# Optimization experiments

Measured on AMD Instinct MI355X. Metric: run time of the kernel, lower is better.

The kernel has to match this reference:

```python
import jax, jax.numpy as jnp
import numpy as np

N, HID, K = 256, 64, 2
B, T_ENC, T_DEC = 64, 12, 12
IN_DIM, OUT_DIM = 2, 1
NUM_SUPPORTS = 2
M = NUM_SUPPORTS * K + 1  # identity + K hops per support


def setup_inputs() -> dict:
    key = jax.random.key(0)
    ks = jax.random.split(key, 16)

    def w(k, shape, scale=0.05):
        return jax.random.normal(k, shape, dtype=jnp.float32) * scale

    def support(k):
        S = jax.random.uniform(k, (N, N), dtype=jnp.float32)
        return S / jnp.sum(S, axis=1, keepdims=True)  # random-walk normalized

    F0e = IN_DIM + HID   # encoder layer-0 concat(input, hidden) feature dim
    F1 = HID + HID       # layer-1 feature dim
    F0d = OUT_DIM + HID  # decoder layer-0 feature dim
    return {
        "encoder_inputs": jax.random.normal(ks[0], (B, T_ENC, N, IN_DIM), dtype=jnp.float32),
        "decoder_inputs": jax.random.normal(ks[1], (B, T_DEC, N, OUT_DIM), dtype=jnp.float32),
        "support0": support(ks[2]),
        "support1": support(ks[3]),
        "enc0_Wg": w(ks[4], (F0e, M, 2 * HID)), "enc0_bg": jnp.ones((2 * HID,), jnp.float32),
        "enc0_Wc": w(ks[5], (F0e, M, HID)),     "enc0_bc": jnp.zeros((HID,), jnp.float32),
        "enc1_Wg": w(ks[6], (F1, M, 2 * HID)),  "enc1_bg": jnp.ones((2 * HID,), jnp.float32),
        "enc1_Wc": w(ks[7], (F1, M, HID)),      "enc1_bc": jnp.zeros((HID,), jnp.float32),
        "dec0_Wg": w(ks[8], (F0d, M, 2 * HID)), "dec0_bg": jnp.ones((2 * HID,), jnp.float32),
        "dec0_Wc": w(ks[9], (F0d, M, HID)),     "dec0_bc": jnp.zeros((HID,), jnp.float32),
        "dec1_Wg": w(ks[10], (F1, M, 2 * HID)), "dec1_bg": jnp.ones((2 * HID,), jnp.float32),
        "dec1_Wc": w(ks[11], (F1, M, HID)),     "dec1_bc": jnp.zeros((HID,), jnp.float32),
        "proj_W": w(ks[12], (HID, OUT_DIM), 0.1),
        "proj_b": jnp.zeros((OUT_DIM,), jnp.float32),
    }


def _diff_conv(supports, x, h, W, b, in_dim):
    # x: (B, N*in_dim), h: (B, N*HID), W: (F, M, O) matching torch flatten order (f*M+m)
    Bsz = x.shape[0]
    xs = jnp.concatenate([x.reshape(Bsz, N, in_dim), h.reshape(Bsz, N, HID)], axis=-1)
    mats = [xs]
    for S in supports:
        x0 = xs
        x1 = jnp.einsum('mn,bnf->bmf', S, xs)
        mats.append(x1)
        for _ in range(2, K + 1):
            x2 = 2.0 * jnp.einsum('mn,bnf->bmf', S, x1) - x0  # Chebyshev recurrence
            mats.append(x2)
            x1, x0 = x2, x1
    X = jnp.stack(mats, axis=2)  # (B, N, M, F)
    out = jnp.einsum('bnmf,fmo->bno', X, W) + b
    return out.reshape(Bsz, -1)


def _cell(supports, x, h, Wg, bg, Wc, bc, in_dim):
    # DCGRUCell: sigmoid gates from diffusion conv, tanh candidate, GRU update
    Bsz = x.shape[0]
    ru = jax.nn.sigmoid(_diff_conv(supports, x, h, Wg, bg, in_dim)).reshape(Bsz, N, 2 * HID)
    r = ru[..., :HID].reshape(Bsz, N * HID)
    u = ru[..., HID:].reshape(Bsz, N * HID)
    c = jnp.tanh(_diff_conv(supports, x, r * h, Wc, bc, in_dim))
    return u * h + (1.0 - u) * c


def _forward(encoder_inputs, decoder_inputs, support0, support1,
             enc0_Wg, enc0_bg, enc0_Wc, enc0_bc, enc1_Wg, enc1_bg, enc1_Wc, enc1_bc,
             dec0_Wg, dec0_bg, dec0_Wc, dec0_bc, dec1_Wg, dec1_bg, dec1_Wc, dec1_bc,
             proj_W, proj_b):
    sup = (support0, support1)
    Bsz = encoder_inputs.shape[0]
    # encoder: (B,T,N,D) -> (T,B,N*D); zero initial hidden
    cur = jnp.transpose(encoder_inputs, (1, 0, 2, 3)).reshape(T_ENC, Bsz, N * IN_DIM)
    enc_params = [(enc0_Wg, enc0_bg, enc0_Wc, enc0_bc, IN_DIM),
                  (enc1_Wg, enc1_bg, enc1_Wc, enc1_bc, HID)]
    h_enc = []
    for (Wg, bg, Wc, bc, ind) in enc_params:
        h0 = jnp.zeros((Bsz, N * HID), cur.dtype)
        def estep(h, x, Wg=Wg, bg=bg, Wc=Wc, bc=bc, ind=ind):
            hn = _cell(sup, x, h, Wg, bg, Wc, bc, ind)
            return hn, hn
        hT, cur = jax.lax.scan(estep, h0, cur)
        h_enc.append(hT)
    # decoder (eval mode: no teacher forcing, dropout off); go symbol = zeros
    dec_params = [(dec0_Wg, dec0_bg, dec0_Wc, dec0_bc, OUT_DIM),
                  (dec1_Wg, dec1_bg, dec1_Wc, dec1_bc, HID)]
    go = jnp.zeros((Bsz, N * OUT_DIM), cur.dtype)

    def dstep(carry, _):
        hs, cur_in = carry
        out = cur_in
        new_hs = []
        for i, (Wg, bg, Wc, bc, ind) in enumerate(dec_params):
            hn = _cell(sup, out, hs[i], Wg, bg, Wc, bc, ind)
            out = hn
            new_hs.append(hn)
        proj = (jnp.einsum('bnh,ho->bno', out.reshape(Bsz, N, HID), proj_W) + proj_b)
        proj = proj.reshape(Bsz, N * OUT_DIM)
        return ((new_hs[0], new_hs[1]), proj), proj

    _, outs = jax.lax.scan(dstep, ((h_enc[0], h_enc[1]), go), None, length=T_DEC)
    outs = outs.reshape(T_DEC, Bsz, N, OUT_DIM)
    return jnp.transpose(outs, (1, 0, 2, 3))  # (B, T_DEC, N, OUT_DIM)


def reference(encoder_inputs, decoder_inputs, support0, support1,
              enc0_Wg, enc0_bg, enc0_Wc, enc0_bc, enc1_Wg, enc1_bg, enc1_Wc, enc1_bc,
              dec0_Wg, dec0_bg, dec0_Wc, dec0_bc, dec1_Wg, dec1_bg, dec1_Wc, dec1_bc,
              proj_W, proj_b):
    return _forward(encoder_inputs, decoder_inputs, support0, support1,
                    enc0_Wg, enc0_bg, enc0_Wc, enc0_bc, enc1_Wg, enc1_bg, enc1_Wc, enc1_bc,
                    dec0_Wg, dec0_bg, dec0_Wc, dec0_bc, dec1_Wg, dec1_bg, dec1_Wc, dec1_bc,
                    proj_W, proj_b)
```

## Files before the change

### kernel.cpp

```cpp
#include <hip/hip_runtime.h>
#include <stdint.h>


typedef short short8 __attribute__((ext_vector_type(8)));
typedef float f32x4 __attribute__((ext_vector_type(4)));
typedef unsigned short ushort4v __attribute__((ext_vector_type(4)));
typedef unsigned long long u64;
typedef u64 u64x2 __attribute__((ext_vector_type(2)));

#define DEVI __device__ __forceinline__

DEVI unsigned short f2bf(float x) {
  unsigned int u = __builtin_bit_cast(unsigned int, x);
  u += 0x7FFFu + ((u >> 16) & 1u);
  return (unsigned short)(u >> 16);
}
DEVI u64 ald(const u64* p) { return __hip_atomic_load(p, __ATOMIC_RELAXED, __HIP_MEMORY_SCOPE_AGENT); }
DEVI void ast(u64* p, u64 v) { __hip_atomic_store(p, v, __ATOMIC_RELAXED, __HIP_MEMORY_SCOPE_AGENT); }
DEVI float aldf(const float* p) { return __hip_atomic_load(p, __ATOMIC_RELAXED, __HIP_MEMORY_SCOPE_AGENT); }
DEVI void astf(float* p, float v) { __hip_atomic_store(p, v, __ATOMIC_RELAXED, __HIP_MEMORY_SCOPE_AGENT); }

struct KP {
  const float* enc_in;
  const float* sup0; const float* sup1;
  const float* Wsrc[8];
  const float* bias[8];
  const float* prW; const float* prB;
  float* out;
  unsigned short* A;
  unsigned short* Wp[8];
  unsigned short* H0[2];
  unsigned short* H1[2];
  unsigned short* RH0;
  unsigned short* RH1;
  float* XD;
  unsigned* ctr;
};

__global__ void prep(KP p) {
  const int i = blockIdx.x, tid = threadIdx.x;
  {
    const int s = i & 1, r = i >> 1;
    const float* S = s ? p.sup1 : p.sup0;
    float acc = 0.f;
    for (int k = 0; k < 256; ++k) acc = fmaf(S[r * 256 + k], S[k * 256 + tid], acc);
    p.A[(2 * s + 0) * 65536 + r * 256 + tid] = f2bf(S[r * 256 + tid]);
    p.A[(2 * s + 1) * 65536 + r * 256 + tid] = f2bf(2.f * acc - (r == tid ? 1.f : 0.f));
  }
  {
    const int gtid = i * 256 + tid;
    const int Fs[8]  = {66, 66, 128, 128, 65, 65, 128, 128};
    const int Os[8]  = {128, 64, 128, 64, 128, 64, 128, 64};
    const int FPs[8] = {96, 96, 128, 128, 96, 96, 128, 128};
    for (int w = 0; w < 8; ++w) {
      const int FPw = FPs[w], KPw = 5 * FPw, tot = Os[w] * KPw;
      for (int e = gtid; e < tot; e += 512 * 256) {
        const int o = e / KPw, k2 = e - o * KPw, m = k2 / FPw, f = k2 - m * FPw;
        p.Wp[w][e] = f2bf((f < Fs[w]) ? p.Wsrc[w][(f * 5 + m) * Os[w] + o] : 0.f);
      }
    }
  }
  {
    const int gtid = i * 256 + tid;
    u64* z0 = (u64*)p.H0[0];
    u64* z1 = (u64*)p.H1[0];
    ast(z0 + 2 * gtid, 0); ast(z0 + 2 * gtid + 1, 0);
    ast(z1 + 2 * gtid, 0); ast(z1 + 2 * gtid + 1, 0);
  }
  if (i == 0 && tid < 64)
    __hip_atomic_store(p.ctr + tid * 64, 0u, __ATOMIC_RELAXED, __HIP_MEMORY_SCOPE_AGENT);
}

template<int IND, int FP, int MODE, bool XSTAGE>
DEVI void dc_stage(int b, int n0, int tid,
                   const float* xf32,
                   const unsigned short* xbf,
                   const unsigned short* hrows,
                   const unsigned short* Amats,
                   const unsigned short* Wp, const float* bias,
                   f32x4 (&hreg)[2], f32x4 (&ureg)[2],
                   unsigned short* grows,
                   const float* projW, const float* projB,
                   float* outp, float* xdout,
                   unsigned short* xsT, unsigned short* Hbuf)
{
  constexpr int O = (MODE == 0) ? 128 : 64;
  constexpr int KPW = 5 * FP;
  constexpr int XS = 264;
  constexpr int HS = 136;
  constexpr int NFT = FP / 16;
  constexpr int NOT_ = O / 16;
  constexpr int FT_W = (NFT + 3) / 4;
  constexpr int OT_W = (NOT_ + 3) / 4;

  const int wv8 = tid >> 6, ln = tid & 63;
  const int l15 = ln & 15, l4 = ln >> 4;
  const int wr = wv8 & 1, wc = wv8 >> 1;
  const int r0 = wr * 32;

  {
    u64 la[4], lb[4];
    const u64* src = (const u64*)hrows;
#pragma unroll
    for (int it = 0; it < 4; ++it) {
      const int g = tid + it * 512;
      la[it] = ald(src + 2 * g); lb[it] = ald(src + 2 * g + 1);
    }
#pragma unroll
    for (int it = 0; it < 4; ++it) {
      const int g = tid + it * 512, row = g >> 5, c = g & 31;
      u64x2 v; v[0] = la[it]; v[1] = lb[it];
      *reinterpret_cast<u64x2*>(&xsT[(IND + row) * XS + c * 8]) = v;
    }
  }
  if (XSTAGE) {
    if (IND == 64) {
      u64 la[4], lb[4];
      const u64* src = (const u64*)xbf;
#pragma unroll
      for (int it = 0; it < 4; ++it) {
        const int g = tid + it * 512;
        la[it] = ald(src + 2 * g); lb[it] = ald(src + 2 * g + 1);
      }
#pragma unroll
      for (int it = 0; it < 4; ++it) {
        const int g = tid + it * 512, row = g >> 5, c = g & 31;
        u64x2 v; v[0] = la[it]; v[1] = lb[it];
        *reinterpret_cast<u64x2*>(&xsT[row * XS + c * 8]) = v;
      }
    } else if (IND == 2) {
      const float v = xf32[tid];
      xsT[(tid & 1) * XS + (tid >> 1)] = f2bf(v);
    } else {
      if (tid < 256) xsT[tid] = xf32 ? f2bf(aldf(xf32 + tid)) : (unsigned short)0;
    }
  }
  __syncthreads();
#pragma unroll
  for (int it = 0; it < FP / 8; ++it) {
    const int e = tid + it * 512, f = e >> 6, nl = e & 63;
    Hbuf[nl * HS + f] = xsT[f * XS + n0 + nl];
  }
  __syncthreads();

  f32x4 pacc[2][OT_W];
#pragma unroll
  for (int rt = 0; rt < 2; ++rt)
#pragma unroll
    for (int oi = 0; oi < OT_W; ++oi) pacc[rt][oi] = 0.f;

  auto proj_step = [&](int m) {
#pragma unroll
    for (int k0 = 0; k0 < FP; k0 += 32) {
      short8 af[2];
#pragma unroll
      for (int rt = 0; rt < 2; ++rt)
        af[rt] = *reinterpret_cast<const short8*>(&Hbuf[(r0 + rt * 16 + l15) * HS + k0 + l4 * 8]);
#pragma unroll
      for (int oi = 0; oi < OT_W; ++oi) {
        const int ot = wc + 4 * oi;
        if (ot < NOT_) {
          short8 bf = *reinterpret_cast<const short8*>(&Wp[(ot * 16 + l15) * KPW + m * FP + k0 + l4 * 8]);
#pragma unroll
          for (int rt = 0; rt < 2; ++rt)
            pacc[rt][oi] = __builtin_amdgcn_mfma_f32_16x16x32_bf16(af[rt], bf, pacc[rt][oi], 0, 0, 0);
        }
      }
    }
  };

  proj_step(0);

  for (int mi = 0; mi < 4; ++mi) {
    const unsigned short* Am = Amats + mi * 65536;
    f32x4 hacc[2][FT_W];
#pragma unroll
    for (int rt = 0; rt < 2; ++rt)
#pragma unroll
      for (int fi = 0; fi < FT_W; ++fi) hacc[rt][fi] = 0.f;

#pragma unroll
    for (int k0 = 0; k0 < 256; k0 += 32) {
      short8 af[2];
#pragma unroll
      for (int rt = 0; rt < 2; ++rt)
        af[rt] = *reinterpret_cast<const short8*>(&Am[(n0 + r0 + rt * 16 + l15) * 256 + k0 + l4 * 8]);
#pragma unroll
      for (int fi = 0; fi < FT_W; ++fi) {
        const int ft = wc + 4 * fi;
        if (ft < NFT) {
          short8 bf = *reinterpret_cast<const short8*>(&xsT[(ft * 16 + l15) * XS + k0 + l4 * 8]);
#pragma unroll
          for (int rt = 0; rt < 2; ++rt)
            hacc[rt][fi] = __builtin_amdgcn_mfma_f32_16x16x32_bf16(af[rt], bf, hacc[rt][fi], 0, 0, 0);
        }
      }
    }
    __syncthreads();
#pragma unroll
    for (int fi = 0; fi < FT_W; ++fi) {
      const int ft = wc + 4 * fi;
      if (ft < NFT) {
#pragma unroll
        for (int rt = 0; rt < 2; ++rt)
#pragma unroll
          for (int j = 0; j < 4; ++j)
            Hbuf[(r0 + rt * 16 + l4 * 4 + j) * HS + ft * 16 + l15] = f2bf(hacc[rt][fi][j]);
      }
    }
    __syncthreads();
    proj_step(mi + 1);
  }

  if (MODE == 0) {
    const float br = bias[wc * 16 + l15];
    const float bu = bias[64 + wc * 16 + l15];
#pragma unroll
    for (int rt = 0; rt < 2; ++rt) {
      f32x4 uu;
      ushort4v pk;
#pragma unroll
      for (int jj = 0; jj < 4; ++jj) {
        const float r = 1.f / (1.f + __expf(-(pacc[rt][0][jj] + br)));
        uu[jj] = 1.f / (1.f + __expf(-(pacc[rt][1][jj] + bu)));
        pk[jj] = f2bf(r * hreg[rt][jj]);
      }
      ureg[rt] = uu;
      ast((u64*)(grows + (wc * 16 + l15) * 256 + n0 + r0 + rt * 16 + l4 * 4),
          __builtin_bit_cast(u64, pk));
    }
  } else {
    float* hrow = reinterpret_cast<float*>(Hbuf);
    if (MODE == 2) __syncthreads();
    const float bc = bias[wc * 16 + l15];
#pragma unroll
    for (int rt = 0; rt < 2; ++rt) {
      f32x4 hn;
      ushort4v pk;
#pragma unroll
      for (int jj = 0; jj < 4; ++jj) {
        const float ex = __expf(2.f * (pacc[rt][0][jj] + bc));
        const float c = 1.f - 2.f / (ex + 1.f);
        hn[jj] = ureg[rt][jj] * hreg[rt][jj] + (1.f - ureg[rt][jj]) * c;
        pk[jj] = f2bf(hn[jj]);
      }
      hreg[rt] = hn;
      ast((u64*)(grows + (wc * 16 + l15) * 256 + n0 + r0 + rt * 16 + l4 * 4),
          __builtin_bit_cast(u64, pk));
      if (MODE == 2) {
#pragma unroll
        for (int jj = 0; jj < 4; ++jj)
          hrow[(r0 + rt * 16 + l4 * 4 + jj) * 68 + wc * 16 + l15] = hn[jj];
      }
    }
    if (MODE == 2) {
      __syncthreads();
      if (tid < 64) {
        float acc = projB[0];
        const float* hr = hrow + tid * 68;
#pragma unroll
        for (int hid = 0; hid < 64; ++hid) acc = fmaf(hr[hid], projW[hid], acc);
        outp[b * 3072 + n0 + tid] = acc;
        astf(xdout + b * 256 + n0 + tid, acc);
      }
    }
  }
}

__launch_bounds__(512, 2)
__global__ void dcrnn_main(KP p) {
  __shared__ __align__(16) unsigned short xsT[128 * 264];
  __shared__ __align__(16) unsigned short Hbuf[64 * 136];
  const int tid = threadIdx.x;
  const int i = (int)blockIdx.x;
  const int q = (i >> 3) & 3;
  const int b = (i & 7) + 8 * (i >> 5);
  const int n0 = q * 64;

  for (int e = tid; e < 128 * 264; e += 512) xsT[e] = 0;
  for (int e = tid; e < 64 * 136; e += 512) Hbuf[e] = 0;
  __syncthreads();

  unsigned* ctr = p.ctr + b * 64;
  unsigned st = 0;
  auto BAR = [&]() {
    ++st;
    asm volatile("s_waitcnt vmcnt(0)" ::: "memory");
    __syncthreads();
    if (tid == 0) {
      __hip_atomic_fetch_add(ctr, 1u, __ATOMIC_RELAXED, __HIP_MEMORY_SCOPE_AGENT);
      const unsigned target = st * 4u;
      while (__hip_atomic_load(ctr, __ATOMIC_RELAXED, __HIP_MEMORY_SCOPE_AGENT) < target)
        __builtin_amdgcn_s_sleep(2);
    }
    __syncthreads();
  };

  f32x4 h0[2], h1[2], u[2];
#pragma unroll
  for (int rt = 0; rt < 2; ++rt) { h0[rt] = 0.f; h1[rt] = 0.f; u[rt] = 0.f; }
  int c0 = 0, c1 = 0;

  for (int t = 0; t < 12; ++t) {
    const float* x0 = p.enc_in + (b * 12 + t) * 512;
    dc_stage<2, 96, 0, true >(b, n0, tid, x0, nullptr, p.H0[c0] + b * 16384, p.A, p.Wp[0], p.bias[0],
                              h0, u, p.RH0 + b * 16384, nullptr, nullptr, nullptr, nullptr, xsT, Hbuf);
    BAR();
    dc_stage<2, 96, 1, false>(b, n0, tid, x0, nullptr, p.RH0 + b * 16384, p.A, p.Wp[1], p.bias[1],
                              h0, u, p.H0[c0 ^ 1] + b * 16384, nullptr, nullptr, nullptr, nullptr, xsT, Hbuf);
    BAR(); c0 ^= 1;
    dc_stage<64, 128, 0, true >(b, n0, tid, nullptr, p.H0[c0] + b * 16384, p.H1[c1] + b * 16384, p.A, p.Wp[2], p.bias[2],
                                h1, u, p.RH1 + b * 16384, nullptr, nullptr, nullptr, nullptr, xsT, Hbuf);
    BAR();
    dc_stage<64, 128, 1, false>(b, n0, tid, nullptr, p.H0[c0] + b * 16384, p.RH1 + b * 16384, p.A, p.Wp[3], p.bias[3],
                                h1, u, p.H1[c1 ^ 1] + b * 16384, nullptr, nullptr, nullptr, nullptr, xsT, Hbuf);
    BAR(); c1 ^= 1;
  }

  for (int t = 0; t < 12; ++t) {
    const float* xd = t ? (p.XD + b * 256) : nullptr;
    dc_stage<1, 96, 0, true >(b, n0, tid, xd, nullptr, p.H0[c0] + b * 16384, p.A, p.Wp[4], p.bias[4],
                              h0, u, p.RH0 + b * 16384, nullptr, nullptr, nullptr, nullptr, xsT, Hbuf);
    BAR();
    dc_stage<1, 96, 1, false>(b, n0, tid, xd, nullptr, p.RH0 + b * 16384, p.A, p.Wp[5], p.bias[5],
                              h0, u, p.H0[c0 ^ 1] + b * 16384, nullptr, nullptr, nullptr, nullptr, xsT, Hbuf);
    BAR(); c0 ^= 1;
    dc_stage<64, 128, 0, true >(b, n0, tid, nullptr, p.H0[c0] + b * 16384, p.H1[c1] + b * 16384, p.A, p.Wp[6], p.bias[6],
                                h1, u, p.RH1 + b * 16384, nullptr, nullptr, nullptr, nullptr, xsT, Hbuf);
    BAR();
    dc_stage<64, 128, 2, false>(b, n0, tid, nullptr, p.H0[c0] + b * 16384, p.RH1 + b * 16384, p.A, p.Wp[7], p.bias[7],
                                h1, u, p.H1[c1 ^ 1] + b * 16384, p.prW, p.prB, p.out + t * 256, p.XD, xsT, Hbuf);
    if (t != 11) BAR();
    c1 ^= 1;
  }
}

extern "C" void kernel_launch(void* const* d_in, const int* in_sizes, int n_in,
                              void* d_out, int out_size, void* d_ws, size_t ws_size,
                              hipStream_t stream)
{
  (void)in_sizes; (void)n_in; (void)out_size; (void)ws_size;
  KP p;
  p.enc_in = (const float*)d_in[0];
  p.sup0 = (const float*)d_in[2];
  p.sup1 = (const float*)d_in[3];
  p.Wsrc[0] = (const float*)d_in[4];  p.bias[0] = (const float*)d_in[5];
  p.Wsrc[1] = (const float*)d_in[6];  p.bias[1] = (const float*)d_in[7];
  p.Wsrc[2] = (const float*)d_in[8];  p.bias[2] = (const float*)d_in[9];
  p.Wsrc[3] = (const float*)d_in[10]; p.bias[3] = (const float*)d_in[11];
  p.Wsrc[4] = (const float*)d_in[12]; p.bias[4] = (const float*)d_in[13];
  p.Wsrc[5] = (const float*)d_in[14]; p.bias[5] = (const float*)d_in[15];
  p.Wsrc[6] = (const float*)d_in[16]; p.bias[6] = (const float*)d_in[17];
  p.Wsrc[7] = (const float*)d_in[18]; p.bias[7] = (const float*)d_in[19];
  p.prW = (const float*)d_in[20];
  p.prB = (const float*)d_in[21];
  p.out = (float*)d_out;

  char* ws = (char*)d_ws;
  size_t off = 0;
  auto carve = [&](size_t bytes) -> char* {
    char* qp = ws + off;
    off += (bytes + 255) & ~(size_t)255;
    return qp;
  };
  p.A = (unsigned short*)carve(4 * 65536 * 2);
  p.Wp[0] = (unsigned short*)carve(128 * 480 * 2);
  p.Wp[1] = (unsigned short*)carve(64 * 480 * 2);
  p.Wp[2] = (unsigned short*)carve(128 * 640 * 2);
  p.Wp[3] = (unsigned short*)carve(64 * 640 * 2);
  p.Wp[4] = (unsigned short*)carve(128 * 480 * 2);
  p.Wp[5] = (unsigned short*)carve(64 * 480 * 2);
  p.Wp[6] = (unsigned short*)carve(128 * 640 * 2);
  p.Wp[7] = (unsigned short*)carve(64 * 640 * 2);
  p.H0[0] = (unsigned short*)carve(64 * 64 * 256 * 2);
  p.H0[1] = (unsigned short*)carve(64 * 64 * 256 * 2);
  p.H1[0] = (unsigned short*)carve(64 * 64 * 256 * 2);
  p.H1[1] = (unsigned short*)carve(64 * 64 * 256 * 2);
  p.RH0 = (unsigned short*)carve(64 * 64 * 256 * 2);
  p.RH1 = (unsigned short*)carve(64 * 64 * 256 * 2);
  p.XD = (float*)carve(64 * 256 * 4);
  p.ctr = (unsigned*)carve(64 * 256);

  prep<<<dim3(512), dim3(256), 0, stream>>>(p);
  dcrnn_main<<<dim3(256), dim3(512), 0, stream>>>(p);
}
```

Before: 2.280 ms.

## Compute all five diffusion terms into separate LDS buffers before projection

The identity term is now handled as a fifth diffusion matrix (a bf16 identity in A5), so all five diffusion products are computed back-to-back into five separate LDS slabs. Projection then runs once over all slabs, which removes the per-hop pair of __syncthreads that used to interleave diffusion and projection. The cost is 256x256 extra MFMA work for the identity matmul and LDS for Hbuf growing from about 17 KB to about 87 KB, which together with xsT (about 68 KB) puts at risk the two-blocks-per-CU occupancy set by the launch bounds.

```diff
diff --git a/kernel.cpp b/kernel.cpp
--- a/kernel.cpp
+++ b/kernel.cpp
@@ -27,7 +27,7 @@
   const float* bias[8];
   const float* prW; const float* prB;
   float* out;
-  unsigned short* A;
+  unsigned short* A5;
   unsigned short* Wp[8];
   unsigned short* H0[2];
   unsigned short* H1[2];
@@ -44,8 +44,9 @@
     const float* S = s ? p.sup1 : p.sup0;
     float acc = 0.f;
     for (int k = 0; k < 256; ++k) acc = fmaf(S[r * 256 + k], S[k * 256 + tid], acc);
-    p.A[(2 * s + 0) * 65536 + r * 256 + tid] = f2bf(S[r * 256 + tid]);
-    p.A[(2 * s + 1) * 65536 + r * 256 + tid] = f2bf(2.f * acc - (r == tid ? 1.f : 0.f));
+    if (s == 0) p.A5[r * 256 + tid] = (r == tid) ? (unsigned short)0x3F80 : (unsigned short)0;
+    p.A5[(1 + 2 * s) * 65536 + r * 256 + tid] = f2bf(S[r * 256 + tid]);
+    p.A5[(2 + 2 * s) * 65536 + r * 256 + tid] = f2bf(2.f * acc - (r == tid ? 1.f : 0.f));
   }
   {
     const int gtid = i * 256 + tid;
@@ -76,7 +77,7 @@
                    const float* xf32,
                    const unsigned short* xbf,
                    const unsigned short* hrows,
-                   const unsigned short* Amats,
+                   const unsigned short* A5,
                    const unsigned short* Wp, const float* bias,
                    f32x4 (&hreg)[2], f32x4 (&ureg)[2],
                    unsigned short* grows,
@@ -88,6 +89,7 @@
   constexpr int KPW = 5 * FP;
   constexpr int XS = 264;
   constexpr int HS = 136;
+  constexpr int HB = 64 * HS;
   constexpr int NFT = FP / 16;
   constexpr int NOT_ = O / 16;
   constexpr int FT_W = (NFT + 3) / 4;
@@ -136,10 +138,44 @@
     }
   }
   __syncthreads();
-#pragma unroll
-  for (int it = 0; it < FP / 8; ++it) {
-    const int e = tid + it * 512, f = e >> 6, nl = e & 63;
-    Hbuf[nl * HS + f] = xsT[f * XS + n0 + nl];
+
+#pragma unroll
+  for (int m = 0; m < 5; ++m) {
+    const unsigned short* Am = A5 + m * 65536;
+    f32x4 hacc[2][FT_W];
+#pragma unroll
+    for (int rt = 0; rt < 2; ++rt)
+#pragma unroll
+      for (int fi = 0; fi < FT_W; ++fi) hacc[rt][fi] = 0.f;
+#pragma unroll
+    for (int k0 = 0; k0 < 256; k0 += 32) {
+      short8 af[2];
+#pragma unroll
+      for (int rt = 0; rt < 2; ++rt)
+        af[rt] = *reinterpret_cast<const short8*>(&Am[(n0 + r0 + rt * 16 + l15) * 256 + k0 + l4 * 8]);
+#pragma unroll
+      for (int fi = 0; fi < FT_W; ++fi) {
+        const int ft = wc + 4 * fi;
+        if (ft < NFT) {
+          short8 bf = *reinterpret_cast<const short8*>(&xsT[(ft * 16 + l15) * XS + k0 + l4 * 8]);
+#pragma unroll
+          for (int rt = 0; rt < 2; ++rt)
+            hacc[rt][fi] = __builtin_amdgcn_mfma_f32_16x16x32_bf16(af[rt], bf, hacc[rt][fi], 0, 0, 0);
+        }
+      }
+    }
+    unsigned short* dst = Hbuf + m * HB;
+#pragma unroll
+    for (int fi = 0; fi < FT_W; ++fi) {
+      const int ft = wc + 4 * fi;
+      if (ft < NFT) {
+#pragma unroll
+        for (int rt = 0; rt < 2; ++rt)
+#pragma unroll
+          for (int j = 0; j < 4; ++j)
+            dst[(r0 + rt * 16 + l4 * 4 + j) * HS + ft * 16 + l15] = f2bf(hacc[rt][fi][j]);
+      }
+    }
   }
   __syncthreads();
 
@@ -148,14 +184,15 @@
   for (int rt = 0; rt < 2; ++rt)
 #pragma unroll
     for (int oi = 0; oi < OT_W; ++oi) pacc[rt][oi] = 0.f;
-
-  auto proj_step = [&](int m) {
+#pragma unroll
+  for (int m = 0; m < 5; ++m) {
+    const unsigned short* hb = Hbuf + m * HB;
 #pragma unroll
     for (int k0 = 0; k0 < FP; k0 += 32) {
       short8 af[2];
 #pragma unroll
       for (int rt = 0; rt < 2; ++rt)
-        af[rt] = *reinterpret_cast<const short8*>(&Hbuf[(r0 + rt * 16 + l15) * HS + k0 + l4 * 8]);
+        af[rt] = *reinterpret_cast<const short8*>(&hb[(r0 + rt * 16 + l15) * HS + k0 + l4 * 8]);
 #pragma unroll
       for (int oi = 0; oi < OT_W; ++oi) {
         const int ot = wc + 4 * oi;
@@ -167,49 +204,6 @@
         }
       }
     }
-  };
-
-  proj_step(0);
-
-  for (int mi = 0; mi < 4; ++mi) {
-    const unsigned short* Am = Amats + mi * 65536;
-    f32x4 hacc[2][FT_W];
-#pragma unroll
-    for (int rt = 0; rt < 2; ++rt)
-#pragma unroll
-      for (int fi = 0; fi < FT_W; ++fi) hacc[rt][fi] = 0.f;
-
-#pragma unroll
-    for (int k0 = 0; k0 < 256; k0 += 32) {
-      short8 af[2];
-#pragma unroll
-      for (int rt = 0; rt < 2; ++rt)
-        af[rt] = *reinterpret_cast<const short8*>(&Am[(n0 + r0 + rt * 16 + l15) * 256 + k0 + l4 * 8]);
-#pragma unroll
-      for (int fi = 0; fi < FT_W; ++fi) {
-        const int ft = wc + 4 * fi;
-        if (ft < NFT) {
-          short8 bf = *reinterpret_cast<const short8*>(&xsT[(ft * 16 + l15) * XS + k0 + l4 * 8]);
-#pragma unroll
-          for (int rt = 0; rt < 2; ++rt)
-            hacc[rt][fi] = __builtin_amdgcn_mfma_f32_16x16x32_bf16(af[rt], bf, hacc[rt][fi], 0, 0, 0);
-        }
-      }
-    }
-    __syncthreads();
-#pragma unroll
-    for (int fi = 0; fi < FT_W; ++fi) {
-      const int ft = wc + 4 * fi;
-      if (ft < NFT) {
-#pragma unroll
-        for (int rt = 0; rt < 2; ++rt)
-#pragma unroll
-          for (int j = 0; j < 4; ++j)
-            Hbuf[(r0 + rt * 16 + l4 * 4 + j) * HS + ft * 16 + l15] = f2bf(hacc[rt][fi][j]);
-      }
-    }
-    __syncthreads();
-    proj_step(mi + 1);
   }
 
   if (MODE == 0) {
@@ -270,7 +264,7 @@
 __launch_bounds__(512, 2)
 __global__ void dcrnn_main(KP p) {
   __shared__ __align__(16) unsigned short xsT[128 * 264];
-  __shared__ __align__(16) unsigned short Hbuf[64 * 136];
+  __shared__ __align__(16) unsigned short Hbuf[5 * 64 * 136];
   const int tid = threadIdx.x;
   const int i = (int)blockIdx.x;
   const int q = (i >> 3) & 3;
@@ -278,7 +272,7 @@
   const int n0 = q * 64;
 
   for (int e = tid; e < 128 * 264; e += 512) xsT[e] = 0;
-  for (int e = tid; e < 64 * 136; e += 512) Hbuf[e] = 0;
+  for (int e = tid; e < 5 * 64 * 136; e += 512) Hbuf[e] = 0;
   __syncthreads();
 
   unsigned* ctr = p.ctr + b * 64;
@@ -303,32 +297,32 @@
 
   for (int t = 0; t < 12; ++t) {
     const float* x0 = p.enc_in + (b * 12 + t) * 512;
-    dc_stage<2, 96, 0, true >(b, n0, tid, x0, nullptr, p.H0[c0] + b * 16384, p.A, p.Wp[0], p.bias[0],
+    dc_stage<2, 96, 0, true >(b, n0, tid, x0, nullptr, p.H0[c0] + b * 16384, p.A5, p.Wp[0], p.bias[0],
                               h0, u, p.RH0 + b * 16384, nullptr, nullptr, nullptr, nullptr, xsT, Hbuf);
     BAR();
-    dc_stage<2, 96, 1, false>(b, n0, tid, x0, nullptr, p.RH0 + b * 16384, p.A, p.Wp[1], p.bias[1],
+    dc_stage<2, 96, 1, false>(b, n0, tid, x0, nullptr, p.RH0 + b * 16384, p.A5, p.Wp[1], p.bias[1],
                               h0, u, p.H0[c0 ^ 1] + b * 16384, nullptr, nullptr, nullptr, nullptr, xsT, Hbuf);
     BAR(); c0 ^= 1;
-    dc_stage<64, 128, 0, true >(b, n0, tid, nullptr, p.H0[c0] + b * 16384, p.H1[c1] + b * 16384, p.A, p.Wp[2], p.bias[2],
+    dc_stage<64, 128, 0, true >(b, n0, tid, nullptr, p.H0[c0] + b * 16384, p.H1[c1] + b * 16384, p.A5, p.Wp[2], p.bias[2],
                                 h1, u, p.RH1 + b * 16384, nullptr, nullptr, nullptr, nullptr, xsT, Hbuf);
     BAR();
-    dc_stage<64, 128, 1, false>(b, n0, tid, nullptr, p.H0[c0] + b * 16384, p.RH1 + b * 16384, p.A, p.Wp[3], p.bias[3],
+    dc_stage<64, 128, 1, false>(b, n0, tid, nullptr, p.H0[c0] + b * 16384, p.RH1 + b * 16384, p.A5, p.Wp[3], p.bias[3],
                                 h1, u, p.H1[c1 ^ 1] + b * 16384, nullptr, nullptr, nullptr, nullptr, xsT, Hbuf);
     BAR(); c1 ^= 1;
   }
 
   for (int t = 0; t < 12; ++t) {
     const float* xd = t ? (p.XD + b * 256) : nullptr;
-    dc_stage<1, 96, 0, true >(b, n0, tid, xd, nullptr, p.H0[c0] + b * 16384, p.A, p.Wp[4], p.bias[4],
+    dc_stage<1, 96, 0, true >(b, n0, tid, xd, nullptr, p.H0[c0] + b * 16384, p.A5, p.Wp[4], p.bias[4],
                               h0, u, p.RH0 + b * 16384, nullptr, nullptr, nullptr, nullptr, xsT, Hbuf);
     BAR();
-    dc_stage<1, 96, 1, false>(b, n0, tid, xd, nullptr, p.RH0 + b * 16384, p.A, p.Wp[5], p.bias[5],
+    dc_stage<1, 96, 1, false>(b, n0, tid, xd, nullptr, p.RH0 + b * 16384, p.A5, p.Wp[5], p.bias[5],
                               h0, u, p.H0[c0 ^ 1] + b * 16384, nullptr, nullptr, nullptr, nullptr, xsT, Hbuf);
     BAR(); c0 ^= 1;
-    dc_stage<64, 128, 0, true >(b, n0, tid, nullptr, p.H0[c0] + b * 16384, p.H1[c1] + b * 16384, p.A, p.Wp[6], p.bias[6],
+    dc_stage<64, 128, 0, true >(b, n0, tid, nullptr, p.H0[c0] + b * 16384, p.H1[c1] + b * 16384, p.A5, p.Wp[6], p.bias[6],
                                 h1, u, p.RH1 + b * 16384, nullptr, nullptr, nullptr, nullptr, xsT, Hbuf);
     BAR();
-    dc_stage<64, 128, 2, false>(b, n0, tid, nullptr, p.H0[c0] + b * 16384, p.RH1 + b * 16384, p.A, p.Wp[7], p.bias[7],
+    dc_stage<64, 128, 2, false>(b, n0, tid, nullptr, p.H0[c0] + b * 16384, p.RH1 + b * 16384, p.A5, p.Wp[7], p.bias[7],
                                 h1, u, p.H1[c1 ^ 1] + b * 16384, p.prW, p.prB, p.out + t * 256, p.XD, xsT, Hbuf);
     if (t != 11) BAR();
     c1 ^= 1;
@@ -363,7 +357,7 @@
     off += (bytes + 255) & ~(size_t)255;
     return qp;
   };
-  p.A = (unsigned short*)carve(4 * 65536 * 2);
+  p.A5 = (unsigned short*)carve(5 * 65536 * 2);
   p.Wp[0] = (unsigned short*)carve(128 * 480 * 2);
   p.Wp[1] = (unsigned short*)carve(64 * 480 * 2);
   p.Wp[2] = (unsigned short*)carve(128 * 640 * 2);
```

Measured after the change: 2.929 ms. 28.5% more time.

## Double-buffer Hbuf to remove per-hop barrier and fuse transpose into staging

Applied to the files above, without the earlier changes.

Hbuf becomes two ping-pong buffers, so the projection MFMA for hop m reads one buffer while hop m+1's diffusion result is written to the other. This drops one __syncthreads per hop and lets the projection overlap the diffusion epilogue. The identity-term transpose into Hbuf is also fused into the global-to-LDS staging loads, removing a separate transpose pass and barrier. The cost is doubled Hbuf LDS (about 35 KB), which may affect the 2-blocks-per-CU occupancy target, plus scattered 2-byte LDS writes during staging.

```diff
diff --git a/kernel.cpp b/kernel.cpp
--- a/kernel.cpp
+++ b/kernel.cpp
@@ -88,6 +88,7 @@
   constexpr int KPW = 5 * FP;
   constexpr int XS = 264;
   constexpr int HS = 136;
+  constexpr int HB = 64 * HS;
   constexpr int NFT = FP / 16;
   constexpr int NOT_ = O / 16;
   constexpr int FT_W = (NFT + 3) / 4;
@@ -111,6 +112,15 @@
       const int g = tid + it * 512, row = g >> 5, c = g & 31;
       u64x2 v; v[0] = la[it]; v[1] = lb[it];
       *reinterpret_cast<u64x2*>(&xsT[(IND + row) * XS + c * 8]) = v;
+      const int c8 = c * 8;
+      if ((unsigned)(c8 - n0) < 64u) {
+        const int nl = c8 - n0;
+#pragma unroll
+        for (int j = 0; j < 4; ++j) {
+          Hbuf[(nl + j) * HS + IND + row]     = (unsigned short)(la[it] >> (16 * j));
+          Hbuf[(nl + 4 + j) * HS + IND + row] = (unsigned short)(lb[it] >> (16 * j));
+        }
+      }
     }
   }
   if (XSTAGE) {
@@ -127,21 +137,42 @@
         const int g = tid + it * 512, row = g >> 5, c = g & 31;
         u64x2 v; v[0] = la[it]; v[1] = lb[it];
         *reinterpret_cast<u64x2*>(&xsT[row * XS + c * 8]) = v;
+        const int c8 = c * 8;
+        if ((unsigned)(c8 - n0) < 64u) {
+          const int nl = c8 - n0;
+#pragma unroll
+          for (int j = 0; j < 4; ++j) {
+            Hbuf[(nl + j) * HS + row]     = (unsigned short)(la[it] >> (16 * j));
+            Hbuf[(nl + 4 + j) * HS + row] = (unsigned short)(lb[it] >> (16 * j));
+          }
+        }
       }
     } else if (IND == 2) {
       const float v = xf32[tid];
-      xsT[(tid & 1) * XS + (tid >> 1)] = f2bf(v);
+      const unsigned short s = f2bf(v);
+      const int n = tid >> 1, f = tid & 1;
+      xsT[f * XS + n] = s;
+      if ((unsigned)(n - n0) < 64u) Hbuf[(n - n0) * HS + f] = s;
     } else {
-      if (tid < 256) xsT[tid] = xf32 ? f2bf(aldf(xf32 + tid)) : (unsigned short)0;
+      if (tid < 256) {
+        const unsigned short s = xf32 ? f2bf(aldf(xf32 + tid)) : (unsigned short)0;
+        xsT[tid] = s;
+        if ((unsigned)(tid - n0) < 64u) Hbuf[(tid - n0) * HS] = s;
+      }
+    }
+  } else {
+    if (IND == 64) {
+      for (int e = tid; e < 64 * 64; e += 512) {
+        const int f = e >> 6, nl = e & 63;
+        Hbuf[nl * HS + f] = xsT[f * XS + n0 + nl];
+      }
+    } else if (IND == 2) {
+      if (tid < 128) Hbuf[(tid >> 1) * HS + (tid & 1)] = xsT[(tid & 1) * XS + n0 + (tid >> 1)];
+    } else {
+      if (tid < 64) Hbuf[tid * HS] = xsT[n0 + tid];
     }
   }
   __syncthreads();
-#pragma unroll
-  for (int it = 0; it < FP / 8; ++it) {
-    const int e = tid + it * 512, f = e >> 6, nl = e & 63;
-    Hbuf[nl * HS + f] = xsT[f * XS + n0 + nl];
-  }
-  __syncthreads();
 
   f32x4 pacc[2][OT_W];
 #pragma unroll
@@ -149,13 +180,13 @@
 #pragma unroll
     for (int oi = 0; oi < OT_W; ++oi) pacc[rt][oi] = 0.f;
 
-  auto proj_step = [&](int m) {
+  auto proj_step = [&](int m, const unsigned short* hb) {
 #pragma unroll
     for (int k0 = 0; k0 < FP; k0 += 32) {
       short8 af[2];
 #pragma unroll
       for (int rt = 0; rt < 2; ++rt)
-        af[rt] = *reinterpret_cast<const short8*>(&Hbuf[(r0 + rt * 16 + l15) * HS + k0 + l4 * 8]);
+        af[rt] = *reinterpret_cast<const short8*>(&hb[(r0 + rt * 16 + l15) * HS + k0 + l4 * 8]);
 #pragma unroll
       for (int oi = 0; oi < OT_W; ++oi) {
         const int ot = wc + 4 * oi;
@@ -169,8 +200,6 @@
     }
   };
 
-  proj_step(0);
-
   for (int mi = 0; mi < 4; ++mi) {
     const unsigned short* Am = Amats + mi * 65536;
     f32x4 hacc[2][FT_W];
@@ -196,7 +225,8 @@
         }
       }
     }
-    __syncthreads();
+    proj_step(mi, Hbuf + (mi & 1) * HB);
+    unsigned short* dst = Hbuf + ((mi + 1) & 1) * HB;
 #pragma unroll
     for (int fi = 0; fi < FT_W; ++fi) {
       const int ft = wc + 4 * fi;
@@ -205,12 +235,12 @@
         for (int rt = 0; rt < 2; ++rt)
 #pragma unroll
           for (int j = 0; j < 4; ++j)
-            Hbuf[(r0 + rt * 16 + l4 * 4 + j) * HS + ft * 16 + l15] = f2bf(hacc[rt][fi][j]);
+            dst[(r0 + rt * 16 + l4 * 4 + j) * HS + ft * 16 + l15] = f2bf(hacc[rt][fi][j]);
       }
     }
     __syncthreads();
-    proj_step(mi + 1);
-  }
+  }
+  proj_step(4, Hbuf);
 
   if (MODE == 0) {
     const float br = bias[wc * 16 + l15];
@@ -230,8 +260,7 @@
           __builtin_bit_cast(u64, pk));
     }
   } else {
-    float* hrow = reinterpret_cast<float*>(Hbuf);
-    if (MODE == 2) __syncthreads();
+    float* hrow = reinterpret_cast<float*>(Hbuf + HB);
     const float bc = bias[wc * 16 + l15];
 #pragma unroll
     for (int rt = 0; rt < 2; ++rt) {
@@ -270,7 +299,7 @@
 __launch_bounds__(512, 2)
 __global__ void dcrnn_main(KP p) {
   __shared__ __align__(16) unsigned short xsT[128 * 264];
-  __shared__ __align__(16) unsigned short Hbuf[64 * 136];
+  __shared__ __align__(16) unsigned short Hbuf[2 * 64 * 136];
   const int tid = threadIdx.x;
   const int i = (int)blockIdx.x;
   const int q = (i >> 3) & 3;
@@ -278,7 +307,7 @@
   const int n0 = q * 64;
 
   for (int e = tid; e < 128 * 264; e += 512) xsT[e] = 0;
-  for (int e = tid; e < 64 * 136; e += 512) Hbuf[e] = 0;
+  for (int e = tid; e < 2 * 64 * 136; e += 512) Hbuf[e] = 0;
   __syncthreads();
 
   unsigned* ctr = p.ctr + b * 64;
```

Result: slower. 2.727 ms (+19.6%).
